# Kernel optimization log

Hardware: AMD Instinct MI355X
Metric: run time of the kernel (lower is better)

## Reference

```python
import jax, jax.numpy as jnp
import numpy as np

# NTM copy-task constants (from ntm_reproduction)
B, T, IN = 2048, 66, 9          # batch, total timesteps, bits+delimiter
H = 100                          # controller LSTM units
N, D = 128, 20                   # memory slots, memory vector dim
OUT = 8                          # output bits
CLIP = 20.0
NUM_HEADS = 2                    # 1 read + 1 write head
PPH = D + 1 + 1 + 3 + 1          # k, beta, g, s(3), gamma = 26 params per head
EPS = 1e-8


def setup_inputs() -> dict:
    key = jax.random.key(0)
    ks = jax.random.split(key, 8)
    s = 0.1
    ctrl_in = IN + D  # input concat with prev read vector
    return {
        "inputs": jax.random.uniform(ks[0], (B, T, IN), dtype=jnp.float32),
        "Wx": jax.random.normal(ks[1], (ctrl_in, 4 * H), dtype=jnp.float32) * s,
        "Wh": jax.random.normal(ks[2], (H, 4 * H), dtype=jnp.float32) * s,
        "b_lstm": jnp.zeros((4 * H,), jnp.float32),
        "W_params": jax.random.normal(ks[3], (H, NUM_HEADS * PPH + 2 * D), dtype=jnp.float32) * s,
        "b_params": jnp.zeros((NUM_HEADS * PPH + 2 * D,), jnp.float32),
        "W_out": jax.random.normal(ks[4], (H + D, OUT), dtype=jnp.float32) * s,
        "b_out": jnp.zeros((OUT,), jnp.float32),
        "sequence_length": 32,
    }


def _ntm_forward(inputs, Wx, Wh, b_lstm, W_params, b_params, W_out, b_out):
    Bt = inputs.shape[0]

    def step(carry, x_t):
        h, c, r, w_prev, M = carry  # w_prev: [B,2,N], M: [B,N,D]
        # --- controller LSTM ---
        ctrl = jnp.concatenate([x_t, r], axis=-1)
        gates = ctrl @ Wx + h @ Wh + b_lstm
        i, f, g, o = jnp.split(gates, 4, axis=-1)
        c = jax.nn.sigmoid(f) * c + jax.nn.sigmoid(i) * jnp.tanh(g)
        h = jax.nn.sigmoid(o) * jnp.tanh(c)
        # --- head parameters ---
        p = jnp.clip(h @ W_params + b_params, -CLIP, CLIP)
        hp = p[:, : NUM_HEADS * PPH].reshape(Bt, NUM_HEADS, PPH)
        k = jnp.tanh(hp[..., :D])                        # [B,2,D]
        beta = jax.nn.softplus(hp[..., D])               # [B,2]
        gg = jax.nn.sigmoid(hp[..., D + 1])              # [B,2]
        s_sh = jax.nn.softmax(hp[..., D + 2 : D + 5], axis=-1)  # [B,2,3]
        gamma = jax.nn.softplus(hp[..., D + 5]) + 1.0    # [B,2]
        # --- content addressing: cosine similarity ---
        kn = jnp.linalg.norm(k, axis=-1, keepdims=True)          # [B,2,1]
        Mn = jnp.linalg.norm(M, axis=-1)                         # [B,N]
        cos = jnp.einsum('bhd,bnd->bhn', k, M) / (kn * Mn[:, None, :] + EPS)
        w_c = jax.nn.softmax(beta[..., None] * cos, axis=-1)     # [B,2,N]
        # --- interpolation gate ---
        w_g = gg[..., None] * w_c + (1.0 - gg[..., None]) * w_prev
        # --- circular convolution shift (shifts -1, 0, +1) ---
        w_t = (s_sh[..., 0:1] * jnp.roll(w_g, -1, axis=-1)
               + s_sh[..., 1:2] * w_g
               + s_sh[..., 2:3] * jnp.roll(w_g, 1, axis=-1))
        # --- sharpening ---
        w_pow = jnp.power(jnp.maximum(w_t, 1e-16), gamma[..., None])
        w = w_pow / jnp.sum(w_pow, axis=-1, keepdims=True)       # [B,2,N]
        w_r, w_w = w[:, 0], w[:, 1]
        # --- read (from pre-write memory) ---
        r_new = jnp.einsum('bn,bnd->bd', w_r, M)
        # --- write: erase then add ---
        e = jax.nn.sigmoid(p[:, NUM_HEADS * PPH : NUM_HEADS * PPH + D])  # [B,D]
        a = jnp.tanh(p[:, NUM_HEADS * PPH + D :])                         # [B,D]
        M = M * (1.0 - w_w[..., None] * e[:, None, :]) + w_w[..., None] * a[:, None, :]
        # --- output ---
        out = jnp.clip(jnp.concatenate([h, r_new], axis=-1) @ W_out + b_out, -CLIP, CLIP)
        return (h, c, r_new, w, M), out

    h0 = jnp.zeros((Bt, H), inputs.dtype)
    c0 = jnp.zeros((Bt, H), inputs.dtype)
    r0 = jnp.zeros((Bt, D), inputs.dtype)
    w0 = jnp.zeros((Bt, NUM_HEADS, N), inputs.dtype).at[:, :, 0].set(1.0)
    M0 = jnp.full((Bt, N, D), 1e-6, inputs.dtype)
    _, outs = jax.lax.scan(step, (h0, c0, r0, w0, M0), jnp.swapaxes(inputs, 0, 1))
    return jnp.swapaxes(outs, 0, 1)  # [B,T,OUT]


def reference(inputs, Wx, Wh, b_lstm, W_params, b_params, W_out, b_out, sequence_length):
    logits = _ntm_forward(inputs, Wx, Wh, b_lstm, W_params, b_params, W_out, b_out)
    return jax.nn.sigmoid(logits[:, sequence_length + 1 :, :])
```

## Files before the change

kernel.cpp:

```cpp
#include <hip/hip_runtime.h>

namespace {

constexpr int B_TOT  = 2048;
constexpr int T_SEQ  = 66;
constexpr int IN_DIM = 9;
constexpr int H      = 100;
constexpr int N      = 128;
constexpr int D      = 20;
constexpr int G      = 4;
constexpr int NTHR   = 512;
constexpr float CLIPV = 20.0f;

constexpr int NCT_BIG = 32;
constexpr int NCT_SM  = 25;
constexpr int WS_BIG_SLOTS = NCT_BIG * 4 * 64;
constexpr int WS_SM_OFF_U16 = WS_BIG_SLOTS * 8;
constexpr int WS_SM_SLOTS = NCT_SM * 64;

constexpr int MT_ROW = 132;
constexpr int MSKT   = D * MT_ROW + 4;

constexpr int HA_STRIDE = 136;
constexpr int HA_LO     = 4 * HA_STRIDE;
constexpr int HA_TOT    = 8 * HA_STRIDE;
constexpr int SA_STRIDE = 40;
constexpr int SA_TOT    = 4 * SA_STRIDE;
constexpr int W_ROW = 132;

constexpr int OFF_M    = 0;
constexpr int OFF_GT   = OFF_M + G * MSKT;
constexpr int OFF_C    = OFF_GT + 2048;
constexpr int OFF_HA   = OFF_C + 400;
constexpr int OFF_SA   = OFF_HA + HA_TOT / 2;
constexpr int OFF_BIAS = OFF_SA + SA_TOT / 2;
constexpr int OFF_R    = OFF_BIAS + 512;
constexpr int OFF_KV   = OFF_R + 80;
constexpr int OFF_SC   = OFF_KV + 160;
constexpr int OFF_EA   = OFF_SC + 64;
constexpr int OFF_W    = OFF_EA + 160;
constexpr int OFF_WO2  = OFF_W + 8 * W_ROW;
constexpr int OFF_OUT  = OFF_WO2 + 160;
constexpr int SMEM_FLOATS = OFF_OUT + 1152;
constexpr int SMEM_BYTES  = SMEM_FLOATS * 4;

typedef __attribute__((ext_vector_type(8))) short bf16x8;
typedef __attribute__((ext_vector_type(4))) float f32x4;

__device__ __forceinline__ float fexp2(float x) { return __builtin_amdgcn_exp2f(x); }
__device__ __forceinline__ float flog2(float x) { return __builtin_amdgcn_logf(x); }
__device__ __forceinline__ float frcp(float x)  { return __builtin_amdgcn_rcpf(x); }
__device__ __forceinline__ float fexp(float x)  { return fexp2(x * 1.4426950408889634f); }
__device__ __forceinline__ float fsig(float x)  { return frcp(1.f + fexp2(-1.4426950408889634f * x)); }
__device__ __forceinline__ float ftanh(float x) { return 1.f - 2.f * frcp(1.f + fexp2(2.8853900817779268f * x)); }
__device__ __forceinline__ float fsoftplus(float x) { return log1pf(fexp(x)); }

__device__ __forceinline__ unsigned short f2bf(float x) {
  unsigned u = __float_as_uint(x);
  u = (u + 0x7FFFu + ((u >> 16) & 1u)) >> 16;
  return (unsigned short)u;
}
__device__ __forceinline__ float bf2f(unsigned short h) {
  return __uint_as_float(((unsigned)h) << 16);
}

template <int C>
__device__ __forceinline__ float dpp_add(float x) {
  return x + __int_as_float(__builtin_amdgcn_mov_dpp(__float_as_int(x), C, 0xF, 0xF, true));
}
__device__ __forceinline__ float qred(float x) { return dpp_add<0x4E>(dpp_add<0xB1>(x)); }

__device__ __forceinline__ void wred_max2(float& a, float& b) {
#pragma unroll
  for (int off = 32; off; off >>= 1) {
    a = fmaxf(a, __shfl_xor(a, off, 64));
    b = fmaxf(b, __shfl_xor(b, off, 64));
  }
}
__device__ __forceinline__ void wred_sum2(float& a, float& b) {
#pragma unroll
  for (int off = 32; off; off >>= 1) {
    a += __shfl_xor(a, off, 64);
    b += __shfl_xor(b, off, 64);
  }
}

__global__ void setup_kernel(unsigned short* __restrict__ ws,
                             const float* __restrict__ Wx, const float* __restrict__ Wh,
                             const float* __restrict__ Wp, const float* __restrict__ Wo) {
  int idx = blockIdx.x * 256 + threadIdx.x;
  if (idx < WS_BIG_SLOTS) {
    int lane = idx & 63, kt = (idx >> 6) & 3, ct = idx >> 8;
    int col = ct * 16 + (lane & 15);
    int k0 = kt * 32 + ((lane >> 4) << 3);
    unsigned short v[8];
#pragma unroll
    for (int j = 0; j < 8; ++j) {
      int k = k0 + j;
      float f = 0.f;
      if (k < 100) {
        if (col < 400) f = Wh[k * 400 + col];
        else if (col < 492) f = Wp[k * 92 + (col - 400)];
        else if (col < 500) f = Wo[k * 8 + (col - 492)];
      }
      v[j] = f2bf(f);
    }
    uint4 pk;
    pk.x = (unsigned)v[0] | ((unsigned)v[1] << 16);
    pk.y = (unsigned)v[2] | ((unsigned)v[3] << 16);
    pk.z = (unsigned)v[4] | ((unsigned)v[5] << 16);
    pk.w = (unsigned)v[6] | ((unsigned)v[7] << 16);
    *(uint4*)(ws + (size_t)idx * 8) = pk;
  } else if (idx < WS_BIG_SLOTS + WS_SM_SLOTS) {
    int s = idx - WS_BIG_SLOTS;
    int lane = s & 63, ct = s >> 6;
    int col = ct * 16 + (lane & 15);
    int k0 = (lane >> 4) << 3;
    unsigned short v[8];
#pragma unroll
    for (int j = 0; j < 8; ++j) {
      int k = k0 + j;
      float f = (k < 29) ? Wx[k * 400 + col] : 0.f;
      v[j] = f2bf(f);
    }
    uint4 pk;
    pk.x = (unsigned)v[0] | ((unsigned)v[1] << 16);
    pk.y = (unsigned)v[2] | ((unsigned)v[3] << 16);
    pk.z = (unsigned)v[4] | ((unsigned)v[5] << 16);
    pk.w = (unsigned)v[6] | ((unsigned)v[7] << 16);
    *(uint4*)(ws + (size_t)(WS_SM_OFF_U16 + (size_t)s * 8)) = pk;
  }
}

__global__ __launch_bounds__(NTHR, 4) void ntm_kernel(
    const float* __restrict__ inputs, const unsigned short* __restrict__ wsu,
    const float* __restrict__ b_lstm, const float* __restrict__ b_params,
    const float* __restrict__ b_out, const float* __restrict__ W_out,
    const int* __restrict__ seqp, float* __restrict__ outp) {
  extern __shared__ float sm[];
  const int tid = threadIdx.x;
  const int lane = tid & 63;
  const int wv = tid >> 6;
  const int b0 = blockIdx.x * G;
  const int tlim = seqp[0] + 1;
  const int TO = T_SEQ - tlim;
  const bool buffered = (TO <= 36);
  unsigned short* hAu = (unsigned short*)(sm + OFF_HA);
  unsigned short* sAu = (unsigned short*)(sm + OFF_SA);
  const bf16x8* wsBig = (const bf16x8*)wsu;
  const bf16x8* wsSm  = (const bf16x8*)(wsu + WS_SM_OFF_U16);

  for (int i = tid; i < G * MSKT; i += NTHR) sm[OFF_M + i] = 1e-6f;
  for (int i = tid; i < 2048; i += NTHR) sm[OFF_GT + i] = 0.f;
  for (int i = tid; i < 400; i += NTHR) sm[OFF_C + i] = 0.f;
  for (int i = tid; i < HA_TOT; i += NTHR) hAu[i] = 0;
  for (int i = tid; i < SA_TOT; i += NTHR) sAu[i] = 0;
  if (tid < 512) {
    float v = 0.f;
    if (tid < 400) v = b_lstm[tid];
    else if (tid < 492) v = b_params[tid - 400];
    else if (tid < 500) v = b_out[tid - 492];
    sm[OFF_BIAS + tid] = v;
  }
  for (int i = tid; i < 80; i += NTHR) sm[OFF_R + i] = 0.f;
  for (int i = tid; i < 8 * W_ROW; i += NTHR)
    sm[OFF_W + i] = ((i % W_ROW) == 0) ? 1.f : 0.f;
  for (int i = tid; i < 160; i += NTHR) sm[OFF_WO2 + i] = W_out[800 + i];
  for (int i = tid; i < 1152; i += NTHR) sm[OFF_OUT + i] = 0.f;
  if (tid >= 448 && tid < 484) {
    int p = tid - 448, g = p / 9, k = p - g * 9;
    sAu[g * SA_STRIDE + k] = f2bf(inputs[(size_t)(b0 + g) * T_SEQ * IN_DIM + k]);
  }
  __syncthreads();

  const int arow = lane & 3;
  const int akoff = (lane >> 4) << 3;

  if (wv < 7) {
    bf16x8 as = *(const bf16x8*)(sAu + arow * SA_STRIDE + akoff);
#pragma unroll
    for (int cti = 0; cti < 4; ++cti) {
      int ct = wv * 4 + cti;
      if (ct < NCT_SM) {
        float bv = sm[OFF_BIAS + ct * 16 + (lane & 15)];
        f32x4 a = {bv, bv, bv, bv};
        a = __builtin_amdgcn_mfma_f32_16x16x32_bf16(as, wsSm[ct * 64 + lane], a, 0, 0, 0);
        if (lane < 16) *(f32x4*)&sm[OFF_GT + (ct * 16 + lane) * 4] = a;
      }
    }
  }
  __syncthreads();

  for (int t = 0; t < T_SEQ; ++t) {
    if (tid < 400) {
      int e = tid >> 2, g = tid & 3;
      float gi = sm[OFF_GT + e * 4 + g];
      float gf = sm[OFF_GT + (100 + e) * 4 + g];
      float gz = sm[OFF_GT + (200 + e) * 4 + g];
      float go = sm[OFF_GT + (300 + e) * 4 + g];
      float c = sm[OFF_C + e * 4 + g];
      float nc = fsig(gf) * c + fsig(gi) * ftanh(gz);
      float h = fsig(go) * ftanh(nc);
      sm[OFF_C + e * 4 + g] = nc;
      unsigned short hh = f2bf(h);
      unsigned short hl = f2bf(h - bf2f(hh));
      hAu[g * HA_STRIDE + e] = hh;
      hAu[HA_LO + g * HA_STRIDE + e] = hl;
    } else if (tid >= 416 && tid < 452) {
      if (t + 1 < T_SEQ) {
        int p = tid - 416, g = p / 9, k = p - g * 9;
        sAu[g * SA_STRIDE + k] =
            f2bf(inputs[((size_t)(b0 + g) * T_SEQ + (t + 1)) * IN_DIM + k]);
      }
    } else if (tid >= 456 && tid < 488) {
      int s = t - 1;
      if (s >= tlim) {
        int u = tid - 456, g = u >> 3, o = u & 7;
        float v = sm[OFF_GT + (492 + o) * 4 + g];
#pragma unroll
        for (int d = 0; d < D; ++d)
          v = fmaf(sm[OFF_R + d * 4 + g], sm[OFF_WO2 + d * 8 + o], v);
        v = fminf(fmaxf(v, -CLIPV), CLIPV);
        v = fsig(v);
        int tp = s - tlim;
        if (buffered) sm[OFF_OUT + (g * TO + tp) * 8 + o] = v;
        else outp[((size_t)(b0 + g) * TO + tp) * 8 + o] = v;
      }
    }
    __syncthreads();

    if (wv < 7) {
      const int ct = 25 + wv;
      float bv = sm[OFF_BIAS + ct * 16 + (lane & 15)];
      f32x4 a = {bv, bv, bv, bv};
#pragma unroll
      for (int kt = 0; kt < 4; ++kt) {
        bf16x8 ahi = *(const bf16x8*)(hAu + arow * HA_STRIDE + kt * 32 + akoff);
        bf16x8 alo = *(const bf16x8*)(hAu + HA_LO + arow * HA_STRIDE + kt * 32 + akoff);
        bf16x8 bf = wsBig[(ct * 4 + kt) * 64 + lane];
        a = __builtin_amdgcn_mfma_f32_16x16x32_bf16(ahi, bf, a, 0, 0, 0);
        a = __builtin_amdgcn_mfma_f32_16x16x32_bf16(alo, bf, a, 0, 0, 0);
      }
      if (lane < 16) {
        int col = ct * 16 + lane;
        if (col < 492) {
          a.x = fminf(fmaxf(a.x, -CLIPV), CLIPV);
          a.y = fminf(fmaxf(a.y, -CLIPV), CLIPV);
          a.z = fminf(fmaxf(a.z, -CLIPV), CLIPV);
          a.w = fminf(fmaxf(a.w, -CLIPV), CLIPV);
        }
        *(f32x4*)&sm[OFF_GT + col * 4] = a;
      }
    }
    __syncthreads();

    if (wv < 4) {
      const int g = wv, l = lane;
      if (l < 40) {
        int hd = l >= 20, j = l - 20 * hd;
        sm[OFF_KV + (2 * g + hd) * 20 + j] =
            ftanh(sm[OFF_GT + (400 + hd * 26 + j) * 4 + g]);
      } else if (l < 52) {
        int hd = (l - 40) >= 6, which = (l - 40) - 6 * hd;
        float v = sm[OFF_GT + (400 + hd * 26 + 20 + which) * 4 + g];
        float* scp = &sm[OFF_SC + (2 * g + hd) * 8];
        if (which == 0) scp[0] = fsoftplus(v);
        else if (which == 1) scp[1] = fsig(v);
        else if (which == 2) {
          float a1 = sm[OFF_GT + (400 + hd * 26 + 23) * 4 + g];
          float a2 = sm[OFF_GT + (400 + hd * 26 + 24) * 4 + g];
          float mx = fmaxf(v, fmaxf(a1, a2));
          float e0 = fexp(v - mx), e1 = fexp(a1 - mx), e2 = fexp(a2 - mx);
          float inv = frcp(e0 + e1 + e2);
          scp[2] = e0 * inv; scp[3] = e1 * inv; scp[4] = e2 * inv;
        } else if (which == 5) {
          scp[5] = fsoftplus(v) + 1.f;
        }
      }
      asm volatile("s_waitcnt lgkmcnt(0)" ::: "memory");
      __builtin_amdgcn_sched_barrier(0);

      const float* Mg = &sm[OFF_M + g * MSKT];
      const float* kv0 = &sm[OFF_KV + (2 * g) * 20];
      const float* kv1 = &sm[OFF_KV + (2 * g + 1) * 20];
      float d00 = 0.f, d01 = 0.f, d10 = 0.f, d11 = 0.f;
      float kn0 = 0.f, kn1 = 0.f, n0s = 0.f, n1s = 0.f;
#pragma unroll
      for (int d = 0; d < D; ++d) {
        float k0 = kv0[d], k1 = kv1[d];
        float m0 = Mg[d * MT_ROW + l], m1 = Mg[d * MT_ROW + 64 + l];
        d00 = fmaf(k0, m0, d00); d01 = fmaf(k0, m1, d01);
        d10 = fmaf(k1, m0, d10); d11 = fmaf(k1, m1, d11);
        kn0 = fmaf(k0, k0, kn0); kn1 = fmaf(k1, k1, kn1);
        n0s = fmaf(m0, m0, n0s); n1s = fmaf(m1, m1, n1s);
      }
      kn0 = sqrtf(kn0); kn1 = sqrtf(kn1);
      float Mn0 = sqrtf(n0s), Mn1 = sqrtf(n1s);
      const float* sc0 = &sm[OFF_SC + (2 * g) * 8];
      const float* sc1 = &sm[OFF_SC + (2 * g + 1) * 8];
      float be0 = sc0[0], be1 = sc1[0];
      float S00 = be0 * d00 * frcp(kn0 * Mn0 + 1e-8f);
      float S01 = be0 * d01 * frcp(kn0 * Mn1 + 1e-8f);
      float S10 = be1 * d10 * frcp(kn1 * Mn0 + 1e-8f);
      float S11 = be1 * d11 * frcp(kn1 * Mn1 + 1e-8f);
      float mx0 = fmaxf(S00, S01), mx1 = fmaxf(S10, S11);
      wred_max2(mx0, mx1);
      float e00 = fexp(S00 - mx0), e01 = fexp(S01 - mx0);
      float e10 = fexp(S10 - mx1), e11 = fexp(S11 - mx1);
      float sum0 = e00 + e01, sum1 = e10 + e11;
      wred_sum2(sum0, sum1);
      float si0 = frcp(sum0), si1 = frcp(sum1);
      float* wpa = &sm[OFF_W + (2 * g) * W_ROW];
      float* wpb = &sm[OFF_W + (2 * g + 1) * W_ROW];
      float gg0 = sc0[1], gg1 = sc1[1];
      float wa0 = wpa[l], wa1 = wpa[64 + l], wb0 = wpb[l], wb1 = wpb[64 + l];
      float wg00 = fmaf(gg0, e00 * si0 - wa0, wa0);
      float wg01 = fmaf(gg0, e01 * si0 - wa1, wa1);
      float wg10 = fmaf(gg1, e10 * si1 - wb0, wb0);
      float wg11 = fmaf(gg1, e11 * si1 - wb1, wb1);
      int lp = (l + 1) & 63, lm = (l + 63) & 63;
      float n00 = __shfl(wg00, lp, 64), n01 = __shfl(wg01, lp, 64);
      float p00 = __shfl(wg00, lm, 64), p01 = __shfl(wg01, lm, 64);
      float a0l0 = __shfl(wg00, 0, 64), a1l0 = __shfl(wg01, 0, 64);
      float a0l63 = __shfl(wg00, 63, 64), a1l63 = __shfl(wg01, 63, 64);
      float nxt00 = (l == 63) ? a1l0 : n00;
      float nxt01 = (l == 63) ? a0l0 : n01;
      float prv00 = (l == 0) ? a1l63 : p00;
      float prv01 = (l == 0) ? a0l63 : p01;
      float n10 = __shfl(wg10, lp, 64), n11 = __shfl(wg11, lp, 64);
      float p10 = __shfl(wg10, lm, 64), p11 = __shfl(wg11, lm, 64);
      float b0l0 = __shfl(wg10, 0, 64), b1l0 = __shfl(wg11, 0, 64);
      float b0l63 = __shfl(wg10, 63, 64), b1l63 = __shfl(wg11, 63, 64);
      float nxt10 = (l == 63) ? b1l0 : n10;
      float nxt11 = (l == 63) ? b0l0 : n11;
      float prv10 = (l == 0) ? b1l63 : p10;
      float prv11 = (l == 0) ? b0l63 : p11;
      float s00 = sc0[2], s01s = sc0[3], s02 = sc0[4], gm0 = sc0[5];
      float s10 = sc1[2], s11s = sc1[3], s12 = sc1[4], gm1 = sc1[5];
      float wt00 = fmaxf(fmaf(s00, nxt00, fmaf(s01s, wg00, s02 * prv00)), 1e-16f);
      float wt01 = fmaxf(fmaf(s00, nxt01, fmaf(s01s, wg01, s02 * prv01)), 1e-16f);
      float wt10 = fmaxf(fmaf(s10, nxt10, fmaf(s11s, wg10, s12 * prv10)), 1e-16f);
      float wt11 = fmaxf(fmaf(s10, nxt11, fmaf(s11s, wg11, s12 * prv11)), 1e-16f);
      float m0m = fmaxf(wt00, wt01), m1m = fmaxf(wt10, wt11);
      wred_max2(m0m, m1m);
      float iv0 = frcp(m0m), iv1 = frcp(m1m);
      float q00 = fexp2(gm0 * flog2(wt00 * iv0));
      float q01 = fexp2(gm0 * flog2(wt01 * iv0));
      float q10 = fexp2(gm1 * flog2(wt10 * iv1));
      float q11 = fexp2(gm1 * flog2(wt11 * iv1));
      float sq0 = q00 + q01, sq1 = q10 + q11;
      wred_sum2(sq0, sq1);
      float pi0 = frcp(sq0), pi1 = frcp(sq1);
      wpa[l] = q00 * pi0; wpa[64 + l] = q01 * pi0;
      wpb[l] = q10 * pi1; wpb[64 + l] = q11 * pi1;
    } else {
      const int wq = wv - 4;
      bf16x8 ahi[4], alo[4];
#pragma unroll
      for (int kt = 0; kt < 4; ++kt) {
        ahi[kt] = *(const bf16x8*)(hAu + arow * HA_STRIDE + kt * 32 + akoff);
        alo[kt] = *(const bf16x8*)(hAu + HA_LO + arow * HA_STRIDE + kt * 32 + akoff);
      }
#pragma unroll
      for (int cti = 0; cti < 7; ++cti) {
        int ct = wq + cti * 4;
        if (ct < NCT_SM) {
          float bv = sm[OFF_BIAS + ct * 16 + (lane & 15)];
          f32x4 a = {bv, bv, bv, bv};
#pragma unroll
          for (int kt = 0; kt < 4; ++kt) {
            bf16x8 bf = wsBig[(ct * 4 + kt) * 64 + lane];
            a = __builtin_amdgcn_mfma_f32_16x16x32_bf16(ahi[kt], bf, a, 0, 0, 0);
            a = __builtin_amdgcn_mfma_f32_16x16x32_bf16(alo[kt], bf, a, 0, 0, 0);
          }
          if (lane < 16) *(f32x4*)&sm[OFF_GT + (ct * 16 + lane) * 4] = a;
        }
      }
    }
    __syncthreads();

    if (tid < 320) {
      int pr = tid >> 2, nq = tid & 3;
      int g = pr / 20, d = pr - g * 20;
      const float* wr = &sm[OFF_W + (2 * g) * W_ROW];
      const float* Md = &sm[OFF_M + g * MSKT + d * MT_ROW];
      float s = 0.f;
#pragma unroll
      for (int i = 0; i < 8; ++i) {
        int n = nq * 4 + i * 16;
        float4 w4 = *(const float4*)(wr + n);
        float4 m4 = *(const float4*)(Md + n);
        s = fmaf(w4.x, m4.x, fmaf(w4.y, m4.y, fmaf(w4.z, m4.z, fmaf(w4.w, m4.w, s))));
      }
      s = qred(s);
      if (nq == 0) {
        sm[OFF_R + d * 4 + g] = s;
        sAu[g * SA_STRIDE + 9 + d] = f2bf(s);
      }
    } else if (tid < 480) {
      int p = tid - 320, g = p / 40, j = p - g * 40;
      float v = sm[OFF_GT + (452 + j) * 4 + g];
      sm[OFF_EA + g * 40 + j] = (j < 20) ? fsig(v) : ftanh(v);
    }
    __syncthreads();

    if (wv < 7) {
      bf16x8 as = *(const bf16x8*)(sAu + arow * SA_STRIDE + akoff);
#pragma unroll
      for (int cti = 0; cti < 4; ++cti) {
        int ct = wv * 4 + cti;
        if (ct < NCT_SM) {
          bf16x8 bs = wsSm[ct * 64 + lane];
          f32x4 c = *(const f32x4*)&sm[OFF_GT + (ct * 16 + (lane & 15)) * 4];
          c = __builtin_amdgcn_mfma_f32_16x16x32_bf16(as, bs, c, 0, 0, 0);
          if (lane < 16) *(f32x4*)&sm[OFF_GT + (ct * 16 + lane) * 4] = c;
        }
      }
    }
    if (tid < 256) {
      int g = tid >> 6, n0 = tid & 63;
      const float* ep = &sm[OFF_EA + g * 40];
      const float* ap = ep + 20;
      float* Mg = &sm[OFF_M + g * MSKT];
#pragma unroll
      for (int h2 = 0; h2 < 2; ++h2) {
        int n = n0 + 64 * h2;
        float ww = sm[OFF_W + (2 * g + 1) * W_ROW + n];
#pragma unroll
        for (int d = 0; d < D; ++d) {
          float mv = Mg[d * MT_ROW + n];
          Mg[d * MT_ROW + n] = fmaf(ww, fmaf(-ep[d], mv, ap[d]), mv);
        }
      }
    }
    __syncthreads();
  }

  if (tid < 32) {
    int s = T_SEQ - 1;
    if (s >= tlim) {
      int g = tid >> 3, o = tid & 7;
      float v = sm[OFF_GT + (492 + o) * 4 + g];
#pragma unroll
      for (int d = 0; d < D; ++d)
        v = fmaf(sm[OFF_R + d * 4 + g], sm[OFF_WO2 + d * 8 + o], v);
      v = fminf(fmaxf(v, -CLIPV), CLIPV);
      v = fsig(v);
      int tp = s - tlim;
      if (buffered) sm[OFF_OUT + (g * TO + tp) * 8 + o] = v;
      else outp[((size_t)(b0 + g) * TO + tp) * 8 + o] = v;
    }
  }
  __syncthreads();
  if (buffered) {
    const int total = G * TO * 8;
    for (int i = tid * 4; i < total; i += NTHR * 4) {
      float4 v = *(const float4*)&sm[OFF_OUT + i];
      *(float4*)&outp[(size_t)blockIdx.x * total + i] = v;
    }
  }
}

}

extern "C" void kernel_launch(void* const* d_in, const int* in_sizes, int n_in,
                              void* d_out, int out_size, void* d_ws, size_t ws_size,
                              hipStream_t stream) {
  (void)in_sizes; (void)n_in; (void)out_size; (void)ws_size;
  const float* inputs   = (const float*)d_in[0];
  const float* Wx       = (const float*)d_in[1];
  const float* Wh       = (const float*)d_in[2];
  const float* b_lstm   = (const float*)d_in[3];
  const float* W_params = (const float*)d_in[4];
  const float* b_params = (const float*)d_in[5];
  const float* W_out    = (const float*)d_in[6];
  const float* b_out    = (const float*)d_in[7];
  const int*   seqp     = (const int*)d_in[8];
  float* out = (float*)d_out;
  unsigned short* wsu = (unsigned short*)d_ws;

  constexpr int SETUP_N = WS_BIG_SLOTS + WS_SM_SLOTS;
  setup_kernel<<<(SETUP_N + 255) / 256, 256, 0, stream>>>(wsu, Wx, Wh, W_params,
                                                          W_out);

  hipFuncSetAttribute((const void*)ntm_kernel,
                      hipFuncAttributeMaxDynamicSharedMemorySize, SMEM_BYTES);
  ntm_kernel<<<B_TOT / G, NTHR, SMEM_BYTES, stream>>>(
      inputs, wsu, b_lstm, b_params, b_out, W_out, seqp, out);
}
```

Baseline: 567.3 us.

## Pack eight batch rows per block and fold hi/lo bf16 split into MFMA rows

Doubles the batch rows per workgroup from 4 to 8 and the threads from 512 to 1024, so each 16-row MFMA tile carries more useful rows. The hi and lo bf16 halves of h now sit in separate A-matrix rows (0-7 and 8-15), so one MFMA per k-tile replaces two and a cross-half shuffle sums them. Shared memory layouts, thread-role ranges and strides are rescaled to match. Costs: larger LDS footprint and 1024-thread blocks lower occupancy, and the grid shrinks to 256 blocks, leaving fewer blocks per CU.

Measured after the change: 1.277 ms. 125% more time.

```diff
diff --git a/kernel.cpp b/kernel.cpp
--- a/kernel.cpp
+++ b/kernel.cpp
@@ -8,13 +8,12 @@
 constexpr int H      = 100;
 constexpr int N      = 128;
 constexpr int D      = 20;
-constexpr int G      = 4;
-constexpr int NTHR   = 512;
+constexpr int G      = 8;
+constexpr int NTHR   = 1024;
 constexpr float CLIPV = 20.0f;
 
-constexpr int NCT_BIG = 32;
 constexpr int NCT_SM  = 25;
-constexpr int WS_BIG_SLOTS = NCT_BIG * 4 * 64;
+constexpr int WS_BIG_SLOTS = 32 * 4 * 64;
 constexpr int WS_SM_OFF_U16 = WS_BIG_SLOTS * 8;
 constexpr int WS_SM_SLOTS = NCT_SM * 64;
 
@@ -22,26 +21,25 @@
 constexpr int MSKT   = D * MT_ROW + 4;
 
 constexpr int HA_STRIDE = 136;
-constexpr int HA_LO     = 4 * HA_STRIDE;
-constexpr int HA_TOT    = 8 * HA_STRIDE;
+constexpr int HA_TOT    = 16 * HA_STRIDE;
 constexpr int SA_STRIDE = 40;
-constexpr int SA_TOT    = 4 * SA_STRIDE;
+constexpr int SA_TOT    = G * SA_STRIDE;
 constexpr int W_ROW = 132;
 
 constexpr int OFF_M    = 0;
 constexpr int OFF_GT   = OFF_M + G * MSKT;
-constexpr int OFF_C    = OFF_GT + 2048;
-constexpr int OFF_HA   = OFF_C + 400;
+constexpr int OFF_C    = OFF_GT + 4096;
+constexpr int OFF_HA   = OFF_C + 800;
 constexpr int OFF_SA   = OFF_HA + HA_TOT / 2;
 constexpr int OFF_BIAS = OFF_SA + SA_TOT / 2;
 constexpr int OFF_R    = OFF_BIAS + 512;
-constexpr int OFF_KV   = OFF_R + 80;
-constexpr int OFF_SC   = OFF_KV + 160;
-constexpr int OFF_EA   = OFF_SC + 64;
-constexpr int OFF_W    = OFF_EA + 160;
-constexpr int OFF_WO2  = OFF_W + 8 * W_ROW;
+constexpr int OFF_KV   = OFF_R + 160;
+constexpr int OFF_SC   = OFF_KV + 320;
+constexpr int OFF_EA   = OFF_SC + 128;
+constexpr int OFF_W    = OFF_EA + 320;
+constexpr int OFF_WO2  = OFF_W + 16 * W_ROW;
 constexpr int OFF_OUT  = OFF_WO2 + 160;
-constexpr int SMEM_FLOATS = OFF_OUT + 1152;
+constexpr int SMEM_FLOATS = OFF_OUT + 2304;
 constexpr int SMEM_BYTES  = SMEM_FLOATS * 4;
 
 typedef __attribute__((ext_vector_type(8))) short bf16x8;
@@ -83,6 +81,15 @@
     a += __shfl_xor(a, off, 64);
     b += __shfl_xor(b, off, 64);
   }
+}
+
+__device__ __forceinline__ f32x4 fold32(f32x4 a) {
+  f32x4 r;
+  r.x = a.x + __shfl_xor(a.x, 32, 64);
+  r.y = a.y + __shfl_xor(a.y, 32, 64);
+  r.z = a.z + __shfl_xor(a.z, 32, 64);
+  r.w = a.w + __shfl_xor(a.w, 32, 64);
+  return r;
 }
 
 __global__ void setup_kernel(unsigned short* __restrict__ ws,
@@ -151,8 +158,8 @@
   const bf16x8* wsSm  = (const bf16x8*)(wsu + WS_SM_OFF_U16);
 
   for (int i = tid; i < G * MSKT; i += NTHR) sm[OFF_M + i] = 1e-6f;
-  for (int i = tid; i < 2048; i += NTHR) sm[OFF_GT + i] = 0.f;
-  for (int i = tid; i < 400; i += NTHR) sm[OFF_C + i] = 0.f;
+  for (int i = tid; i < 4096; i += NTHR) sm[OFF_GT + i] = 0.f;
+  for (int i = tid; i < 800; i += NTHR) sm[OFF_C + i] = 0.f;
   for (int i = tid; i < HA_TOT; i += NTHR) hAu[i] = 0;
   for (int i = tid; i < SA_TOT; i += NTHR) sAu[i] = 0;
   if (tid < 512) {
@@ -162,64 +169,67 @@
     else if (tid < 500) v = b_out[tid - 492];
     sm[OFF_BIAS + tid] = v;
   }
-  for (int i = tid; i < 80; i += NTHR) sm[OFF_R + i] = 0.f;
-  for (int i = tid; i < 8 * W_ROW; i += NTHR)
+  for (int i = tid; i < 160; i += NTHR) sm[OFF_R + i] = 0.f;
+  for (int i = tid; i < 16 * W_ROW; i += NTHR)
     sm[OFF_W + i] = ((i % W_ROW) == 0) ? 1.f : 0.f;
   for (int i = tid; i < 160; i += NTHR) sm[OFF_WO2 + i] = W_out[800 + i];
-  for (int i = tid; i < 1152; i += NTHR) sm[OFF_OUT + i] = 0.f;
-  if (tid >= 448 && tid < 484) {
-    int p = tid - 448, g = p / 9, k = p - g * 9;
+  for (int i = tid; i < 2304; i += NTHR) sm[OFF_OUT + i] = 0.f;
+  if (tid >= 896 && tid < 896 + G * IN_DIM) {
+    int p = tid - 896, g = p / 9, k = p - g * 9;
     sAu[g * SA_STRIDE + k] = f2bf(inputs[(size_t)(b0 + g) * T_SEQ * IN_DIM + k]);
   }
   __syncthreads();
 
-  const int arow = lane & 3;
   const int akoff = (lane >> 4) << 3;
+  const int arow16 = lane & 15;
+  const int arow8 = lane & 7;
+  const int ccol = lane & 15;
+  const int crow4 = (lane >> 4) << 2;
 
   if (wv < 7) {
-    bf16x8 as = *(const bf16x8*)(sAu + arow * SA_STRIDE + akoff);
+    bf16x8 as = *(const bf16x8*)(sAu + arow8 * SA_STRIDE + akoff);
 #pragma unroll
     for (int cti = 0; cti < 4; ++cti) {
       int ct = wv * 4 + cti;
       if (ct < NCT_SM) {
-        float bv = sm[OFF_BIAS + ct * 16 + (lane & 15)];
+        float bv = (lane < 32) ? sm[OFF_BIAS + ct * 16 + ccol] : 0.f;
         f32x4 a = {bv, bv, bv, bv};
         a = __builtin_amdgcn_mfma_f32_16x16x32_bf16(as, wsSm[ct * 64 + lane], a, 0, 0, 0);
-        if (lane < 16) *(f32x4*)&sm[OFF_GT + (ct * 16 + lane) * 4] = a;
+        if (lane < 32) *(f32x4*)&sm[OFF_GT + (ct * 16 + ccol) * 8 + crow4] = a;
       }
     }
   }
   __syncthreads();
 
   for (int t = 0; t < T_SEQ; ++t) {
-    if (tid < 400) {
-      int e = tid >> 2, g = tid & 3;
-      float gi = sm[OFF_GT + e * 4 + g];
-      float gf = sm[OFF_GT + (100 + e) * 4 + g];
-      float gz = sm[OFF_GT + (200 + e) * 4 + g];
-      float go = sm[OFF_GT + (300 + e) * 4 + g];
-      float c = sm[OFF_C + e * 4 + g];
+    if (tid < 800) {
+      int e = tid >> 3, g = tid & 7;
+      float gi = sm[OFF_GT + e * 8 + g];
+      float gf = sm[OFF_GT + (100 + e) * 8 + g];
+      float gz = sm[OFF_GT + (200 + e) * 8 + g];
+      float go = sm[OFF_GT + (300 + e) * 8 + g];
+      float c = sm[OFF_C + e * 8 + g];
       float nc = fsig(gf) * c + fsig(gi) * ftanh(gz);
       float h = fsig(go) * ftanh(nc);
-      sm[OFF_C + e * 4 + g] = nc;
+      sm[OFF_C + e * 8 + g] = nc;
       unsigned short hh = f2bf(h);
       unsigned short hl = f2bf(h - bf2f(hh));
       hAu[g * HA_STRIDE + e] = hh;
-      hAu[HA_LO + g * HA_STRIDE + e] = hl;
-    } else if (tid >= 416 && tid < 452) {
+      hAu[(g + 8) * HA_STRIDE + e] = hl;
+    } else if (tid >= 832 && tid < 832 + G * IN_DIM) {
       if (t + 1 < T_SEQ) {
-        int p = tid - 416, g = p / 9, k = p - g * 9;
+        int p = tid - 832, g = p / 9, k = p - g * 9;
         sAu[g * SA_STRIDE + k] =
             f2bf(inputs[((size_t)(b0 + g) * T_SEQ + (t + 1)) * IN_DIM + k]);
       }
-    } else if (tid >= 456 && tid < 488) {
+    } else if (tid >= 960) {
       int s = t - 1;
       if (s >= tlim) {
-        int u = tid - 456, g = u >> 3, o = u & 7;
-        float v = sm[OFF_GT + (492 + o) * 4 + g];
+        int u = tid - 960, g = u >> 3, o = u & 7;
+        float v = sm[OFF_GT + (492 + o) * 8 + g];
 #pragma unroll
         for (int d = 0; d < D; ++d)
-          v = fmaf(sm[OFF_R + d * 4 + g], sm[OFF_WO2 + d * 8 + o], v);
+          v = fmaf(sm[OFF_R + d * 8 + g], sm[OFF_WO2 + d * 8 + o], v);
         v = fminf(fmaxf(v, -CLIPV), CLIPV);
         v = fsig(v);
         int tp = s - tlim;
@@ -231,44 +241,42 @@
 
     if (wv < 7) {
       const int ct = 25 + wv;
-      float bv = sm[OFF_BIAS + ct * 16 + (lane & 15)];
+      float bv = (lane < 32) ? sm[OFF_BIAS + ct * 16 + ccol] : 0.f;
       f32x4 a = {bv, bv, bv, bv};
 #pragma unroll
       for (int kt = 0; kt < 4; ++kt) {
-        bf16x8 ahi = *(const bf16x8*)(hAu + arow * HA_STRIDE + kt * 32 + akoff);
-        bf16x8 alo = *(const bf16x8*)(hAu + HA_LO + arow * HA_STRIDE + kt * 32 + akoff);
-        bf16x8 bf = wsBig[(ct * 4 + kt) * 64 + lane];
-        a = __builtin_amdgcn_mfma_f32_16x16x32_bf16(ahi, bf, a, 0, 0, 0);
-        a = __builtin_amdgcn_mfma_f32_16x16x32_bf16(alo, bf, a, 0, 0, 0);
-      }
-      if (lane < 16) {
-        int col = ct * 16 + lane;
+        bf16x8 af = *(const bf16x8*)(hAu + arow16 * HA_STRIDE + kt * 32 + akoff);
+        a = __builtin_amdgcn_mfma_f32_16x16x32_bf16(af, wsBig[(ct * 4 + kt) * 64 + lane], a, 0, 0, 0);
+      }
+      f32x4 sfold = fold32(a);
+      if (lane < 32) {
+        int col = ct * 16 + ccol;
         if (col < 492) {
-          a.x = fminf(fmaxf(a.x, -CLIPV), CLIPV);
-          a.y = fminf(fmaxf(a.y, -CLIPV), CLIPV);
-          a.z = fminf(fmaxf(a.z, -CLIPV), CLIPV);
-          a.w = fminf(fmaxf(a.w, -CLIPV), CLIPV);
+          sfold.x = fminf(fmaxf(sfold.x, -CLIPV), CLIPV);
+          sfold.y = fminf(fmaxf(sfold.y, -CLIPV), CLIPV);
+          sfold.z = fminf(fmaxf(sfold.z, -CLIPV), CLIPV);
+          sfold.w = fminf(fmaxf(sfold.w, -CLIPV), CLIPV);
         }
-        *(f32x4*)&sm[OFF_GT + col * 4] = a;
+        *(f32x4*)&sm[OFF_GT + col * 8 + crow4] = sfold;
       }
     }
     __syncthreads();
 
-    if (wv < 4) {
+    if (wv < 8) {
       const int g = wv, l = lane;
       if (l < 40) {
         int hd = l >= 20, j = l - 20 * hd;
         sm[OFF_KV + (2 * g + hd) * 20 + j] =
-            ftanh(sm[OFF_GT + (400 + hd * 26 + j) * 4 + g]);
+            ftanh(sm[OFF_GT + (400 + hd * 26 + j) * 8 + g]);
       } else if (l < 52) {
         int hd = (l - 40) >= 6, which = (l - 40) - 6 * hd;
-        float v = sm[OFF_GT + (400 + hd * 26 + 20 + which) * 4 + g];
+        float v = sm[OFF_GT + (400 + hd * 26 + 20 + which) * 8 + g];
         float* scp = &sm[OFF_SC + (2 * g + hd) * 8];
         if (which == 0) scp[0] = fsoftplus(v);
         else if (which == 1) scp[1] = fsig(v);
         else if (which == 2) {
-          float a1 = sm[OFF_GT + (400 + hd * 26 + 23) * 4 + g];
-          float a2 = sm[OFF_GT + (400 + hd * 26 + 24) * 4 + g];
+          float a1 = sm[OFF_GT + (400 + hd * 26 + 23) * 8 + g];
+          float a2 = sm[OFF_GT + (400 + hd * 26 + 24) * 8 + g];
           float mx = fmaxf(v, fmaxf(a1, a2));
           float e0 = fexp(v - mx), e1 = fexp(a1 - mx), e2 = fexp(a2 - mx);
           float inv = frcp(e0 + e1 + e2);
@@ -354,32 +362,30 @@
       wpa[l] = q00 * pi0; wpa[64 + l] = q01 * pi0;
       wpb[l] = q10 * pi1; wpb[64 + l] = q11 * pi1;
     } else {
-      const int wq = wv - 4;
-      bf16x8 ahi[4], alo[4];
-#pragma unroll
-      for (int kt = 0; kt < 4; ++kt) {
-        ahi[kt] = *(const bf16x8*)(hAu + arow * HA_STRIDE + kt * 32 + akoff);
-        alo[kt] = *(const bf16x8*)(hAu + HA_LO + arow * HA_STRIDE + kt * 32 + akoff);
-      }
-#pragma unroll
-      for (int cti = 0; cti < 7; ++cti) {
-        int ct = wq + cti * 4;
+      const int wq = wv - 8;
+      bf16x8 af[4];
+#pragma unroll
+      for (int kt = 0; kt < 4; ++kt)
+        af[kt] = *(const bf16x8*)(hAu + arow16 * HA_STRIDE + kt * 32 + akoff);
+#pragma unroll
+      for (int cti = 0; cti < 4; ++cti) {
+        int ct = wq + cti * 8;
         if (ct < NCT_SM) {
-          float bv = sm[OFF_BIAS + ct * 16 + (lane & 15)];
+          float bv = (lane < 32) ? sm[OFF_BIAS + ct * 16 + ccol] : 0.f;
           f32x4 a = {bv, bv, bv, bv};
 #pragma unroll
-          for (int kt = 0; kt < 4; ++kt) {
-            bf16x8 bf = wsBig[(ct * 4 + kt) * 64 + lane];
-            a = __builtin_amdgcn_mfma_f32_16x16x32_bf16(ahi[kt], bf, a, 0, 0, 0);
-            a = __builtin_amdgcn_mfma_f32_16x16x32_bf16(alo[kt], bf, a, 0, 0, 0);
-          }
-          if (lane < 16) *(f32x4*)&sm[OFF_GT + (ct * 16 + lane) * 4] = a;
+          for (int kt = 0; kt < 4; ++kt)
+            a = __builtin_amdgcn_mfma_f32_16x16x32_bf16(
+                af[kt], wsBig[(ct * 4 + kt) * 64 + lane], a, 0, 0, 0);
+          f32x4 sfold = fold32(a);
+          if (lane < 32)
+            *(f32x4*)&sm[OFF_GT + (ct * 16 + ccol) * 8 + crow4] = sfold;
         }
       }
     }
     __syncthreads();
 
-    if (tid < 320) {
+    if (tid < 640) {
       int pr = tid >> 2, nq = tid & 3;
       int g = pr / 20, d = pr - g * 20;
       const float* wr = &sm[OFF_W + (2 * g) * W_ROW];
@@ -394,31 +400,32 @@
       }
       s = qred(s);
       if (nq == 0) {
-        sm[OFF_R + d * 4 + g] = s;
+        sm[OFF_R + d * 8 + g] = s;
         sAu[g * SA_STRIDE + 9 + d] = f2bf(s);
       }
-    } else if (tid < 480) {
-      int p = tid - 320, g = p / 40, j = p - g * 40;
-      float v = sm[OFF_GT + (452 + j) * 4 + g];
+    } else if (tid < 960) {
+      int p = tid - 640, g = p / 40, j = p - g * 40;
+      float v = sm[OFF_GT + (452 + j) * 8 + g];
       sm[OFF_EA + g * 40 + j] = (j < 20) ? fsig(v) : ftanh(v);
     }
     __syncthreads();
 
     if (wv < 7) {
-      bf16x8 as = *(const bf16x8*)(sAu + arow * SA_STRIDE + akoff);
+      bf16x8 as = *(const bf16x8*)(sAu + arow8 * SA_STRIDE + akoff);
 #pragma unroll
       for (int cti = 0; cti < 4; ++cti) {
         int ct = wv * 4 + cti;
         if (ct < NCT_SM) {
           bf16x8 bs = wsSm[ct * 64 + lane];
-          f32x4 c = *(const f32x4*)&sm[OFF_GT + (ct * 16 + (lane & 15)) * 4];
+          f32x4 c = {0.f, 0.f, 0.f, 0.f};
+          if (lane < 32) c = *(const f32x4*)&sm[OFF_GT + (ct * 16 + ccol) * 8 + crow4];
           c = __builtin_amdgcn_mfma_f32_16x16x32_bf16(as, bs, c, 0, 0, 0);
-          if (lane < 16) *(f32x4*)&sm[OFF_GT + (ct * 16 + lane) * 4] = c;
+          if (lane < 32) *(f32x4*)&sm[OFF_GT + (ct * 16 + ccol) * 8 + crow4] = c;
         }
       }
-    }
-    if (tid < 256) {
-      int g = tid >> 6, n0 = tid & 63;
+    } else if (tid >= 512) {
+      int slot = tid - 512;
+      int g = slot >> 6, n0 = slot & 63;
       const float* ep = &sm[OFF_EA + g * 40];
       const float* ap = ep + 20;
       float* Mg = &sm[OFF_M + g * MSKT];
@@ -436,14 +443,14 @@
     __syncthreads();
   }
 
-  if (tid < 32) {
+  if (tid < 64) {
     int s = T_SEQ - 1;
     if (s >= tlim) {
       int g = tid >> 3, o = tid & 7;
-      float v = sm[OFF_GT + (492 + o) * 4 + g];
+      float v = sm[OFF_GT + (492 + o) * 8 + g];
 #pragma unroll
       for (int d = 0; d < D; ++d)
-        v = fmaf(sm[OFF_R + d * 4 + g], sm[OFF_WO2 + d * 8 + o], v);
+        v = fmaf(sm[OFF_R + d * 8 + g], sm[OFF_WO2 + d * 8 + o], v);
       v = fminf(fmaxf(v, -CLIPV), CLIPV);
       v = fsig(v);
       int tp = s - tlim;
```

## Cache memory row norms during write update and rebalance MFMA/update waves

Applied to the files above, without the earlier changes.

The memory write-update now runs on waves 4-7 using float4 accesses, two threads per column split across the D dimension. It also computes each row's L2 norm and stores it in a new shared buffer, so the content-addressing step no longer recomputes the norms. The small MFMA is moved onto waves 0-3 with its first B fragment prefetched before the barrier, and LDS strides are padded. The cost is extra shared memory and a tighter split of work between waves.

After: 659.9 us. 1.16x slower.

```diff
diff --git a/kernel.cpp b/kernel.cpp
--- a/kernel.cpp
+++ b/kernel.cpp
@@ -12,19 +12,18 @@
 constexpr int NTHR   = 512;
 constexpr float CLIPV = 20.0f;
 
-constexpr int NCT_BIG = 32;
 constexpr int NCT_SM  = 25;
-constexpr int WS_BIG_SLOTS = NCT_BIG * 4 * 64;
+constexpr int WS_BIG_SLOTS = 32 * 4 * 64;
 constexpr int WS_SM_OFF_U16 = WS_BIG_SLOTS * 8;
 constexpr int WS_SM_SLOTS = NCT_SM * 64;
 
-constexpr int MT_ROW = 132;
+constexpr int MT_ROW = 140;
 constexpr int MSKT   = D * MT_ROW + 4;
 
-constexpr int HA_STRIDE = 136;
+constexpr int HA_STRIDE = 144;
 constexpr int HA_LO     = 4 * HA_STRIDE;
 constexpr int HA_TOT    = 8 * HA_STRIDE;
-constexpr int SA_STRIDE = 40;
+constexpr int SA_STRIDE = 48;
 constexpr int SA_TOT    = 4 * SA_STRIDE;
 constexpr int W_ROW = 132;
 
@@ -38,7 +37,8 @@
 constexpr int OFF_KV   = OFF_R + 80;
 constexpr int OFF_SC   = OFF_KV + 160;
 constexpr int OFF_EA   = OFF_SC + 64;
-constexpr int OFF_W    = OFF_EA + 160;
+constexpr int OFF_MN   = OFF_EA + 160;
+constexpr int OFF_W    = OFF_MN + 512;
 constexpr int OFF_WO2  = OFF_W + 8 * W_ROW;
 constexpr int OFF_OUT  = OFF_WO2 + 160;
 constexpr int SMEM_FLOATS = OFF_OUT + 1152;
@@ -163,6 +163,7 @@
     sm[OFF_BIAS + tid] = v;
   }
   for (int i = tid; i < 80; i += NTHR) sm[OFF_R + i] = 0.f;
+  for (int i = tid; i < 512; i += NTHR) sm[OFF_MN + i] = 4.47213595e-6f;
   for (int i = tid; i < 8 * W_ROW; i += NTHR)
     sm[OFF_W + i] = ((i % W_ROW) == 0) ? 1.f : 0.f;
   for (int i = tid; i < 160; i += NTHR) sm[OFF_WO2 + i] = W_out[800 + i];
@@ -284,7 +285,7 @@
       const float* kv0 = &sm[OFF_KV + (2 * g) * 20];
       const float* kv1 = &sm[OFF_KV + (2 * g + 1) * 20];
       float d00 = 0.f, d01 = 0.f, d10 = 0.f, d11 = 0.f;
-      float kn0 = 0.f, kn1 = 0.f, n0s = 0.f, n1s = 0.f;
+      float kn0 = 0.f, kn1 = 0.f;
 #pragma unroll
       for (int d = 0; d < D; ++d) {
         float k0 = kv0[d], k1 = kv1[d];
@@ -292,10 +293,10 @@
         d00 = fmaf(k0, m0, d00); d01 = fmaf(k0, m1, d01);
         d10 = fmaf(k1, m0, d10); d11 = fmaf(k1, m1, d11);
         kn0 = fmaf(k0, k0, kn0); kn1 = fmaf(k1, k1, kn1);
-        n0s = fmaf(m0, m0, n0s); n1s = fmaf(m1, m1, n1s);
       }
       kn0 = sqrtf(kn0); kn1 = sqrtf(kn1);
-      float Mn0 = sqrtf(n0s), Mn1 = sqrtf(n1s);
+      float Mn0 = sm[OFF_MN + g * N + l];
+      float Mn1 = sm[OFF_MN + g * N + 64 + l];
       const float* sc0 = &sm[OFF_SC + (2 * g) * 8];
       const float* sc1 = &sm[OFF_SC + (2 * g + 1) * 8];
       float be0 = sc0[0], be1 = sc1[0];
@@ -379,6 +380,8 @@
     }
     __syncthreads();
 
+    bf16x8 wS0;
+    if (wv < 4) wS0 = wsSm[wv * 64 + lane];
     if (tid < 320) {
       int pr = tid >> 2, nq = tid & 3;
       int g = pr / 20, d = pr - g * 20;
@@ -404,33 +407,53 @@
     }
     __syncthreads();
 
-    if (wv < 7) {
+    if (wv < 4) {
       bf16x8 as = *(const bf16x8*)(sAu + arow * SA_STRIDE + akoff);
 #pragma unroll
-      for (int cti = 0; cti < 4; ++cti) {
-        int ct = wv * 4 + cti;
+      for (int i = 0; i < 7; ++i) {
+        int ct = wv + 4 * i;
         if (ct < NCT_SM) {
-          bf16x8 bs = wsSm[ct * 64 + lane];
+          bf16x8 bs = (i == 0) ? wS0 : wsSm[ct * 64 + lane];
           f32x4 c = *(const f32x4*)&sm[OFF_GT + (ct * 16 + (lane & 15)) * 4];
           c = __builtin_amdgcn_mfma_f32_16x16x32_bf16(as, bs, c, 0, 0, 0);
           if (lane < 16) *(f32x4*)&sm[OFF_GT + (ct * 16 + lane) * 4] = c;
         }
       }
-    }
-    if (tid < 256) {
-      int g = tid >> 6, n0 = tid & 63;
+    } else {
+      int slot = tid - 256;
+      int g = slot >> 6;
+      int rest = slot & 63;
+      int n4 = (rest >> 1) << 2;
+      int dh = rest & 1;
       const float* ep = &sm[OFF_EA + g * 40];
       const float* ap = ep + 20;
       float* Mg = &sm[OFF_M + g * MSKT];
-#pragma unroll
-      for (int h2 = 0; h2 < 2; ++h2) {
-        int n = n0 + 64 * h2;
-        float ww = sm[OFF_W + (2 * g + 1) * W_ROW + n];
-#pragma unroll
-        for (int d = 0; d < D; ++d) {
-          float mv = Mg[d * MT_ROW + n];
-          Mg[d * MT_ROW + n] = fmaf(ww, fmaf(-ep[d], mv, ap[d]), mv);
-        }
+      float4 ww4 = *(const float4*)&sm[OFF_W + (2 * g + 1) * W_ROW + n4];
+      float4 nrm = {0.f, 0.f, 0.f, 0.f};
+#pragma unroll
+      for (int dd = 0; dd < 10; ++dd) {
+        int d = dh * 10 + dd;
+        float ed = ep[d], ad = ap[d];
+        float4 m4 = *(const float4*)(Mg + d * MT_ROW + n4);
+        m4.x = fmaf(ww4.x, fmaf(-ed, m4.x, ad), m4.x);
+        m4.y = fmaf(ww4.y, fmaf(-ed, m4.y, ad), m4.y);
+        m4.z = fmaf(ww4.z, fmaf(-ed, m4.z, ad), m4.z);
+        m4.w = fmaf(ww4.w, fmaf(-ed, m4.w, ad), m4.w);
+        *(float4*)(Mg + d * MT_ROW + n4) = m4;
+        nrm.x = fmaf(m4.x, m4.x, nrm.x);
+        nrm.y = fmaf(m4.y, m4.y, nrm.y);
+        nrm.z = fmaf(m4.z, m4.z, nrm.z);
+        nrm.w = fmaf(m4.w, m4.w, nrm.w);
+      }
+      nrm.x = dpp_add<0xB1>(nrm.x);
+      nrm.y = dpp_add<0xB1>(nrm.y);
+      nrm.z = dpp_add<0xB1>(nrm.z);
+      nrm.w = dpp_add<0xB1>(nrm.w);
+      if (dh == 0) {
+        float4 r4;
+        r4.x = sqrtf(nrm.x); r4.y = sqrtf(nrm.y);
+        r4.z = sqrtf(nrm.z); r4.w = sqrtf(nrm.w);
+        *(float4*)&sm[OFF_MN + g * N + n4] = r4;
       }
     }
     __syncthreads();
```
